# Kernel tuning notes

Hardware: AMD Instinct MI355X
Metric: run time of the kernel (lower is better)

The kernel has to match this reference:

```python
import jax, jax.numpy as jnp
import numpy as np

N, E, IN_DIM, HID, PROJ, NG = 50000, 1600000, 128, 128, 128, 64


def setup_inputs() -> dict:
    key = jax.random.key(0)
    ks = jax.random.split(key, 12)
    def glorot(k, fan_in, fan_out):
        s = (6.0 / (fan_in + fan_out)) ** 0.5
        return jax.random.uniform(k, (fan_in, fan_out), jnp.float32, -s, s)
    x = jax.random.normal(ks[0], (N, IN_DIM), jnp.float32)
    edge_index = jax.random.randint(ks[1], (2, E), 0, N, jnp.int32)
    batch = jnp.sort(jax.random.randint(ks[2], (N,), 0, NG, jnp.int32))
    return {
        "x": x,
        "edge_index": edge_index,
        "batch": batch,
        "num_graphs": NG,
        "W1": glorot(ks[3], IN_DIM, HID), "b1": jnp.zeros((HID,), jnp.float32),
        "W2": glorot(ks[4], HID, HID),    "b2": jnp.zeros((HID,), jnp.float32),
        "pW1": glorot(ks[5], HID, HID),   "pb1": jnp.zeros((HID,), jnp.float32),
        "pW2": glorot(ks[6], HID, PROJ),  "pb2": jnp.zeros((PROJ,), jnp.float32),
    }


def _gcn_norm(edge_index, n_nodes):
    # add self loops, compute symmetric normalization (PyG GCNConv default)
    loop = jnp.arange(n_nodes, dtype=edge_index.dtype)
    src = jnp.concatenate([edge_index[0], loop])
    dst = jnp.concatenate([edge_index[1], loop])
    deg = jax.ops.segment_sum(jnp.ones_like(dst, jnp.float32), dst, num_segments=n_nodes)
    dinv = jnp.where(deg > 0, jax.lax.rsqrt(deg), 0.0)
    norm = dinv[src] * dinv[dst]  # [E+N]
    return src, dst, norm


def _gcn_conv(h, W, b, src, dst, norm, n_nodes):
    hw = h @ W                              # [N, out]
    msg = hw[src] * norm[:, None]           # gather + scale, [E+N, out]
    out = jax.ops.segment_sum(msg, dst, num_segments=n_nodes)  # scatter-add
    return out + b


def reference(x, edge_index, batch, num_graphs, W1, b1, W2, b2, pW1, pb1, pW2, pb2):
    n_nodes = x.shape[0]
    src, dst, norm = _gcn_norm(edge_index, n_nodes)
    # conv stack (dropout is identity in eval mode)
    h = jax.nn.relu(_gcn_conv(x, W1, b1, src, dst, norm, n_nodes))
    h = jax.nn.relu(_gcn_conv(h, W2, b2, src, dst, norm, n_nodes))
    # global mean pool over graphs
    sums = jax.ops.segment_sum(h, batch, num_segments=num_graphs)
    cnts = jax.ops.segment_sum(jnp.ones((n_nodes,), h.dtype), batch, num_segments=num_graphs)
    hg = sums / jnp.maximum(cnts, 1.0)[:, None]
    # MLP projection head
    z = jax.nn.relu(hg @ pW1 + pb1) @ pW2 + pb2
    # L2 normalize (torch F.normalize with eps=1e-12)
    nrm = jnp.maximum(jnp.linalg.norm(z, axis=1, keepdims=True), 1e-12)
    return z / nrm
```

## Files before the change

### kernel.cpp

```cpp
#include <hip/hip_runtime.h>
#include <cstdint>
#include <cstddef>


using short8 = __attribute__((ext_vector_type(8))) short;
using f32x4v = __attribute__((ext_vector_type(4))) float;


static __device__ __forceinline__ unsigned f2bf_rne(float f) {
    unsigned u = __float_as_uint(f);
    return (u + 0x7FFFu + ((u >> 16) & 1u)) >> 16;
}
static __device__ __forceinline__ unsigned pack_bf2(float lo, float hi) {
    return f2bf_rne(lo) | (f2bf_rne(hi) << 16);
}
static __device__ __forceinline__ float bf_lo(unsigned v) {
    return __uint_as_float(v << 16);
}
static __device__ __forceinline__ float bf_hi(unsigned v) {
    return __uint_as_float(v & 0xFFFF0000u);
}


__global__ void k_bincount(const int* __restrict__ dst, int* __restrict__ bcnt,
                           int E, int NB) {
    __shared__ int h[256];
    int t = threadIdx.x;
    h[t] = 0;
    __syncthreads();
    int base_i = blockIdx.x * 4096;
#pragma unroll
    for (int j = 0; j < 16; ++j) {
        int i = base_i + j * 256 + t;
        if (i < E) atomicAdd(&h[dst[i] >> 8], 1);
    }
    __syncthreads();
    if (t < NB && h[t]) atomicAdd(&bcnt[t], h[t]);
}

__global__ void k_bscan(const int* __restrict__ bcnt, int* __restrict__ bbase,
                        int* __restrict__ bcur, int NB,
                        float* __restrict__ pooled, int* __restrict__ cnt,
                        unsigned* __restrict__ hwdummy, int NG) {
    __shared__ int s[256];
    int t = threadIdx.x;
    int v = (t < NB) ? bcnt[t] : 0;
    s[t] = v;
    __syncthreads();
    for (int d = 1; d < 256; d <<= 1) {
        int x = (t >= d) ? s[t - d] : 0;
        __syncthreads();
        s[t] += x;
        __syncthreads();
    }
    if (t < NB) {
        int excl = s[t] - v;
        bbase[t] = excl;
        bcur[t]  = excl;
        if (t == NB - 1) bbase[NB] = s[t];
    }
    float4 z4 = {0.f, 0.f, 0.f, 0.f};
    int n4 = NG * 32;
    for (int i = t; i < n4; i += 256)
        reinterpret_cast<float4*>(pooled)[i] = z4;
    if (t < NG) cnt[t] = 0;
    if (t < 64) hwdummy[t] = 0u;
}


__global__ void k_bin(const int* __restrict__ src, const int* __restrict__ dst,
                      int* __restrict__ bcur, int* __restrict__ bkt,
                      int E, int NB) {
    __shared__ int cnt[256];
    __shared__ int pos[256];
    int t = threadIdx.x;
    int base_i = blockIdx.x * 4096;

    cnt[t] = 0;
    __syncthreads();

    int b_[16];
    int v_[16];
#pragma unroll
    for (int j = 0; j < 16; ++j) {
        int i = base_i + j * 256 + t;
        if (i < E) {
            int s = src[i], d = dst[i];
            v_[j] = s | ((d & 255) << 16);
            int b = d >> 8;
            b_[j] = b;
            atomicAdd(&cnt[b], 1);
        } else {
            b_[j] = -1;
        }
    }
    __syncthreads();

    if (t < NB) {
        int c = cnt[t];
        pos[t] = c ? atomicAdd(&bcur[t], c) : 0;
    }
    __syncthreads();

#pragma unroll
    for (int j = 0; j < 16; ++j) {
        if (b_[j] >= 0) {
            int p = atomicAdd(&pos[b_[j]], 1);
            bkt[p] = v_[j];
        }
    }
}


__global__ void k_fill2(const int* __restrict__ bkt, const int* __restrict__ bbase,
                        int* __restrict__ off, float* __restrict__ dinv,
                        int* __restrict__ csr, int N, int E, int NB) {
    __shared__ int hist[256];
    __shared__ int loff[256];
    __shared__ int cur[256];
    int b = blockIdx.x, t = threadIdx.x;
    if (t < 256) hist[t] = 0;
    __syncthreads();

    int e0 = bbase[b], e1 = bbase[b + 1];
    for (int i = e0 + t; i < e1; i += 1024)
        atomicAdd(&hist[(bkt[i] >> 16) & 255], 1);
    __syncthreads();

    if (t < 256) loff[t] = hist[t];
    __syncthreads();
    for (int d = 1; d < 256; d <<= 1) {
        int x = 0;
        if (t < 256 && t >= d) x = loff[t - d];
        __syncthreads();
        if (t < 256) loff[t] += x;
        __syncthreads();
    }

    if (t < 256) {
        int n = (b << 8) + t;
        if (n < N) {
            int base = e0 + loff[t] - hist[t];
            off[n]  = base;
            cur[t]  = base;
            dinv[n] = rsqrtf((float)(hist[t] + 1));
        }
    }
    if (b == NB - 1 && t == 0) off[N] = E;
    __syncthreads();

    for (int i = e0 + t; i < e1; i += 1024) {
        int v  = bkt[i];
        int dl = (v >> 16) & 255;
        int p  = atomicAdd(&cur[dl], 1);
        csr[p] = v & 0xFFFF;
    }
}


template<bool BF16IN>
__global__ __launch_bounds__(256) void k_gemm(
        const void* __restrict__ in_, const float* __restrict__ W,
        const float* __restrict__ dinv, unsigned* __restrict__ outbf, int N) {
    __shared__ unsigned short wbf[128 * 136];

    int t = threadIdx.x;
    int w  = t >> 6;
    int l  = t & 63;
    int lo = l & 15;
    int hi = l >> 4;

#pragma unroll
    for (int i = 0; i < 16; ++i) {
        int idx = (i * 256 + t) * 4;
        float4 wv = *reinterpret_cast<const float4*>(W + idx);
        int k = idx >> 7, c = idx & 127;
        wbf[(c    ) * 136 + k] = (unsigned short)f2bf_rne(wv.x);
        wbf[(c + 1) * 136 + k] = (unsigned short)f2bf_rne(wv.y);
        wbf[(c + 2) * 136 + k] = (unsigned short)f2bf_rne(wv.z);
        wbf[(c + 3) * 136 + k] = (unsigned short)f2bf_rne(wv.w);
    }
    __syncthreads();

    unsigned short* outS = (unsigned short*)outbf;

#pragma unroll
    for (int tt = 0; tt < 2; ++tt) {
        int rbase = (blockIdx.x * 2 + tt) * 64 + w * 16;
        if (rbase >= N) continue;
        int row  = rbase + lo;
        int rowc = (row < N) ? row : (N - 1);

        short8 a[4];
        if constexpr (BF16IN) {
            const uint4* pu = (const uint4*)in_;
#pragma unroll
            for (int ks = 0; ks < 4; ++ks)
                a[ks] = __builtin_bit_cast(short8, pu[(size_t)rowc * 16 + ks * 4 + hi]);
        } else {
            const float4* pf = (const float4*)in_;
#pragma unroll
            for (int ks = 0; ks < 4; ++ks) {
                float4 fA = pf[(size_t)rowc * 32 + ks * 8 + hi * 2];
                float4 fB = pf[(size_t)rowc * 32 + ks * 8 + hi * 2 + 1];
                short8 s;
                s[0] = (short)f2bf_rne(fA.x); s[1] = (short)f2bf_rne(fA.y);
                s[2] = (short)f2bf_rne(fA.z); s[3] = (short)f2bf_rne(fA.w);
                s[4] = (short)f2bf_rne(fB.x); s[5] = (short)f2bf_rne(fB.y);
                s[6] = (short)f2bf_rne(fB.z); s[7] = (short)f2bf_rne(fB.w);
                a[ks] = s;
            }
        }

        f32x4v acc[8];
#pragma unroll
        for (int i = 0; i < 8; ++i) acc[i] = (f32x4v){0.f, 0.f, 0.f, 0.f};

#pragma unroll
        for (int cp = 0; cp < 2; ++cp) {
            short8 b[4][4];
#pragma unroll
            for (int ct = 0; ct < 4; ++ct) {
                int col = cp * 64 + ct * 16 + lo;
#pragma unroll
                for (int ks = 0; ks < 4; ++ks)
                    b[ct][ks] = *reinterpret_cast<const short8*>(
                        &wbf[col * 136 + ks * 32 + hi * 8]);
            }
#pragma unroll
            for (int ks = 0; ks < 4; ++ks)
#pragma unroll
                for (int ct = 0; ct < 4; ++ct)
                    acc[cp * 4 + ct] = __builtin_amdgcn_mfma_f32_16x16x32_bf16(
                        b[ct][ks], a[ks], acc[cp * 4 + ct], 0, 0, 0);
        }

        if (row < N) {
            float d = dinv[row];
#pragma unroll
            for (int i = 0; i < 8; ++i) {
                int colb = (i >> 2) * 64 + (i & 3) * 16 + hi * 4;
                uint2 o = { pack_bf2(acc[i][0] * d, acc[i][1] * d),
                            pack_bf2(acc[i][2] * d, acc[i][3] * d) };
                *reinterpret_cast<uint2*>(&outS[(size_t)row * 128 + colb]) = o;
            }
        }
    }
}


__global__ void k_aggr(const unsigned* __restrict__ hw, const int* __restrict__ off,
                       const int* __restrict__ csr, const float* __restrict__ dinv,
                       const float* __restrict__ bias, unsigned* __restrict__ out, int N) {
    int wid  = (blockIdx.x * blockDim.x + threadIdx.x) >> 6;
    int lane = threadIdx.x & 63;
    if (wid >= N) return;
    int n  = wid;
    int q  = lane >> 4;
    int li = lane & 15;

    const uint4* hw4 = reinterpret_cast<const uint4*>(hw);

    float a0 = 0.f, a1 = 0.f, a2 = 0.f, a3 = 0.f;
    float a4 = 0.f, a5 = 0.f, a6 = 0.f, a7 = 0.f;
    if (q == 0) {
        uint4 v = hw4[(unsigned)(n << 4) + li];
        a0 = bf_lo(v.x); a1 = bf_hi(v.x);
        a2 = bf_lo(v.y); a3 = bf_hi(v.y);
        a4 = bf_lo(v.z); a5 = bf_hi(v.z);
        a6 = bf_lo(v.w); a7 = bf_hi(v.w);
    }

#define ACC8(v) \
    a0 += bf_lo(v.x); a1 += bf_hi(v.x); \
    a2 += bf_lo(v.y); a3 += bf_hi(v.y); \
    a4 += bf_lo(v.z); a5 += bf_hi(v.z); \
    a6 += bf_lo(v.w); a7 += bf_hi(v.w);

    int e = off[n], e1 = off[n + 1];
    while (e < e1) {
        int rem = e1 - e;
        int cnt = rem < 64 ? rem : 64;
        int s_l = N;
        if (lane < cnt) s_l = csr[e + lane];
        int jn = (cnt + 3) >> 2;
        int j = 0;
        for (; j + 8 <= jn; j += 8) {
            int s0 = __shfl(s_l, 4 * j + q);
            int s1 = __shfl(s_l, 4 * j + 4 + q);
            int s2 = __shfl(s_l, 4 * j + 8 + q);
            int s3 = __shfl(s_l, 4 * j + 12 + q);
            int s4 = __shfl(s_l, 4 * j + 16 + q);
            int s5 = __shfl(s_l, 4 * j + 20 + q);
            int s6 = __shfl(s_l, 4 * j + 24 + q);
            int s7 = __shfl(s_l, 4 * j + 28 + q);
            uint4 v0 = hw4[(unsigned)(s0 << 4) + li];
            uint4 v1 = hw4[(unsigned)(s1 << 4) + li];
            uint4 v2 = hw4[(unsigned)(s2 << 4) + li];
            uint4 v3 = hw4[(unsigned)(s3 << 4) + li];
            uint4 v4 = hw4[(unsigned)(s4 << 4) + li];
            uint4 v5 = hw4[(unsigned)(s5 << 4) + li];
            uint4 v6 = hw4[(unsigned)(s6 << 4) + li];
            uint4 v7 = hw4[(unsigned)(s7 << 4) + li];
            ACC8(v0) ACC8(v1) ACC8(v2) ACC8(v3)
            ACC8(v4) ACC8(v5) ACC8(v6) ACC8(v7)
        }
        for (; j + 4 <= jn; j += 4) {
            int s0 = __shfl(s_l, 4 * j + q);
            int s1 = __shfl(s_l, 4 * j + 4 + q);
            int s2 = __shfl(s_l, 4 * j + 8 + q);
            int s3 = __shfl(s_l, 4 * j + 12 + q);
            uint4 v0 = hw4[(unsigned)(s0 << 4) + li];
            uint4 v1 = hw4[(unsigned)(s1 << 4) + li];
            uint4 v2 = hw4[(unsigned)(s2 << 4) + li];
            uint4 v3 = hw4[(unsigned)(s3 << 4) + li];
            ACC8(v0) ACC8(v1) ACC8(v2) ACC8(v3)
        }
        for (; j < jn; ++j) {
            int   s = __shfl(s_l, 4 * j + q);
            uint4 v = hw4[(unsigned)(s << 4) + li];
            ACC8(v)
        }
        e += cnt;
    }
#undef ACC8

    int p1 = (lane + 32) & 63;
    a0 += __shfl(a0, p1); a1 += __shfl(a1, p1);
    a2 += __shfl(a2, p1); a3 += __shfl(a3, p1);
    a4 += __shfl(a4, p1); a5 += __shfl(a5, p1);
    a6 += __shfl(a6, p1); a7 += __shfl(a7, p1);
    int p2 = (lane + 16) & 63;
    a0 += __shfl(a0, p2); a1 += __shfl(a1, p2);
    a2 += __shfl(a2, p2); a3 += __shfl(a3, p2);
    a4 += __shfl(a4, p2); a5 += __shfl(a5, p2);
    a6 += __shfl(a6, p2); a7 += __shfl(a7, p2);

    if (q == 0) {
        float di = dinv[n];
        const float4* b4 = reinterpret_cast<const float4*>(bias);
        float4 bA = b4[2 * li], bB = b4[2 * li + 1];
        a0 = fmaxf(fmaf(a0, di, bA.x), 0.f); a1 = fmaxf(fmaf(a1, di, bA.y), 0.f);
        a2 = fmaxf(fmaf(a2, di, bA.z), 0.f); a3 = fmaxf(fmaf(a3, di, bA.w), 0.f);
        a4 = fmaxf(fmaf(a4, di, bB.x), 0.f); a5 = fmaxf(fmaf(a5, di, bB.y), 0.f);
        a6 = fmaxf(fmaf(a6, di, bB.z), 0.f); a7 = fmaxf(fmaf(a7, di, bB.w), 0.f);
        uint4 r = { pack_bf2(a0, a1), pack_bf2(a2, a3),
                    pack_bf2(a4, a5), pack_bf2(a6, a7) };
        reinterpret_cast<uint4*>(out)[(unsigned)(n << 4) + li] = r;
    }
}


__global__ void k_pool(const unsigned* __restrict__ h, const int* __restrict__ batch,
                       float* __restrict__ pooled, int* __restrict__ cnt,
                       int N, int npw) {
    int wid  = (blockIdx.x * blockDim.x + threadIdx.x) >> 6;
    int lane = threadIdx.x & 63;
    int n0 = wid * npw;
    if (n0 >= N) return;
    int n1 = n0 + npw; if (n1 > N) n1 = N;

    float ax = 0.f, ay = 0.f;
    int g = batch[n0];
    int c = 0;
    for (int n = n0; n < n1; ++n) {
        int gn = batch[n];
        if (gn != g) {
            atomicAdd(&pooled[g * 128 + 2 * lane],     ax);
            atomicAdd(&pooled[g * 128 + 2 * lane + 1], ay);
            if (lane == 0) atomicAdd(&cnt[g], c);
            ax = 0.f; ay = 0.f; c = 0; g = gn;
        }
        unsigned v = h[(size_t)n * 64 + lane];
        ax += bf_lo(v); ay += bf_hi(v); ++c;
    }
    atomicAdd(&pooled[g * 128 + 2 * lane],     ax);
    atomicAdd(&pooled[g * 128 + 2 * lane + 1], ay);
    if (lane == 0) atomicAdd(&cnt[g], c);
}


__global__ void k_head(const float* __restrict__ pooled, const int* __restrict__ cnt,
                       const float* __restrict__ pW1, const float* __restrict__ pb1,
                       const float* __restrict__ pW2, const float* __restrict__ pb2,
                       float* __restrict__ out) {
    __shared__ float hg[128];
    __shared__ float z1[128];
    __shared__ float red[128];
    int g = blockIdx.x, t = threadIdx.x;

    float c = fmaxf((float)cnt[g], 1.0f);
    hg[t] = pooled[g * 128 + t] / c;
    __syncthreads();

    float a = pb1[t];
#pragma unroll 8
    for (int k = 0; k < 128; ++k) a = fmaf(hg[k], pW1[k * 128 + t], a);
    z1[t] = fmaxf(a, 0.f);
    __syncthreads();

    float z = pb2[t];
#pragma unroll 8
    for (int k = 0; k < 128; ++k) z = fmaf(z1[k], pW2[k * 128 + t], z);

    red[t] = z * z;
    __syncthreads();
    for (int d = 64; d > 0; d >>= 1) {
        if (t < d) red[t] += red[t + d];
        __syncthreads();
    }
    float nrm = fmaxf(sqrtf(red[0]), 1e-12f);
    out[g * 128 + t] = z / nrm;
}


extern "C" void kernel_launch(void* const* d_in, const int* in_sizes, int n_in,
                              void* d_out, int out_size, void* d_ws, size_t ws_size,
                              hipStream_t stream) {
    const float* x    = (const float*)d_in[0];
    const int*   eidx = (const int*)  d_in[1];
    const int*   batch= (const int*)  d_in[2];
    const float* W1   = (const float*)d_in[4];
    const float* b1   = (const float*)d_in[5];
    const float* W2   = (const float*)d_in[6];
    const float* b2   = (const float*)d_in[7];
    const float* pW1  = (const float*)d_in[8];
    const float* pb1  = (const float*)d_in[9];
    const float* pW2  = (const float*)d_in[10];
    const float* pb2  = (const float*)d_in[11];
    float* out = (float*)d_out;

    const int N  = in_sizes[0] / 128;
    const int E  = in_sizes[1] / 2;
    const int NG = out_size / 128;
    const int NB = (N + 255) >> 8;

    const int* src = eidx;
    const int* dst = eidx + E;

    char* p = (char*)d_ws;
    auto alloc = [&](size_t bytes) -> void* {
        void* r = (void*)p;
        p += (bytes + 255) & ~(size_t)255;
        return r;
    };
    int*      bcnt     = (int*)     alloc((size_t)NB * 4);
    int*      cnt      = (int*)     alloc((size_t)NG * 4);
    float*    pooled   = (float*)   alloc((size_t)NG * 128 * 4);
    int*      bbase    = (int*)     alloc((size_t)(NB + 1) * 4);
    int*      bcur     = (int*)     alloc((size_t)NB * 4);
    int*      off      = (int*)     alloc((size_t)(N + 1) * 4);
    float*    dinv     = (float*)   alloc((size_t)N * 4);
    int*      bkt      = (int*)     alloc((size_t)E * 4);
    int*      csr      = (int*)     alloc((size_t)E * 4);
    unsigned* bufH     = (unsigned*)alloc((size_t)(N + 1) * 64 * 4);
    unsigned* bufB     = (unsigned*)alloc((size_t)N * 64 * 4);
    (void)ws_size;

    const int tB = (E + 4095) / 4096;

    hipMemsetAsync(bcnt, 0, (size_t)NB * 4, stream);

    k_bincount<<<tB, 256, 0, stream>>>(dst, bcnt, E, NB);
    k_bscan   <<<1, 256, 0, stream>>>(bcnt, bbase, bcur, NB,
                                      pooled, cnt, bufH + (size_t)N * 64, NG);
    k_bin     <<<tB, 256, 0, stream>>>(src, dst, bcur, bkt, E, NB);
    k_fill2   <<<NB, 1024, 0, stream>>>(bkt, bbase, off, dinv, csr, N, E, NB);

    const int nrt = (N + 63) / 64;
    const int gB  = (nrt + 1) / 2;
    const int aB  = (N + 3) / 4;

    k_gemm<false><<<gB, 256, 0, stream>>>((const void*)x, W1, dinv, bufH, N);
    k_aggr<<<aB, 256, 0, stream>>>(bufH, off, csr, dinv, b1, bufB, N);
    k_gemm<true><<<gB, 256, 0, stream>>>((const void*)bufB, W2, dinv, bufH, N);
    k_aggr<<<aB, 256, 0, stream>>>(bufH, off, csr, dinv, b2, bufB, N);

    const int NPW = 32;
    const int waves = (N + NPW - 1) / NPW;
    const int pB = (waves * 64 + 255) / 256;
    k_pool<<<pB, 256, 0, stream>>>(bufB, batch, pooled, cnt, N, NPW);

    k_head<<<NG, 128, 0, stream>>>(pooled, cnt, pW1, pb1, pW2, pb2, out);
}
```

Measured before the change: 220.9 us.

## Privatize per-wave LDS histograms and fuse mean pooling into head kernel

The binning, bucket-fill and CSR-fill kernels now give each wave (or each 256-thread group) its own shared-memory histogram and cursor array, to reduce contention on shared atomics. The pooling kernel and its zero-initialisation are removed. Each head block now binary-searches the sorted batch array for its graph's node range and sums that range itself, with no global float atomics and one fewer launch. In exchange, pooling runs on only 64 blocks, each walking about 780 nodes serially, which may expose memory latency. The fused path also assumes batch is sorted.

```diff
diff --git a/kernel.cpp b/kernel.cpp
--- a/kernel.cpp
+++ b/kernel.cpp
@@ -24,24 +24,30 @@
 
 __global__ void k_bincount(const int* __restrict__ dst, int* __restrict__ bcnt,
                            int E, int NB) {
-    __shared__ int h[256];
+    __shared__ int h4[4][256];
     int t = threadIdx.x;
-    h[t] = 0;
+    int w = t >> 6;
+    ((int*)h4)[t]       = 0;
+    ((int*)h4)[t + 256] = 0;
+    ((int*)h4)[t + 512] = 0;
+    ((int*)h4)[t + 768] = 0;
     __syncthreads();
     int base_i = blockIdx.x * 4096;
 #pragma unroll
     for (int j = 0; j < 16; ++j) {
         int i = base_i + j * 256 + t;
-        if (i < E) atomicAdd(&h[dst[i] >> 8], 1);
-    }
-    __syncthreads();
-    if (t < NB && h[t]) atomicAdd(&bcnt[t], h[t]);
+        if (i < E) atomicAdd(&h4[w][dst[i] >> 8], 1);
+    }
+    __syncthreads();
+    if (t < NB) {
+        int s = h4[0][t] + h4[1][t] + h4[2][t] + h4[3][t];
+        if (s) atomicAdd(&bcnt[t], s);
+    }
 }
 
 __global__ void k_bscan(const int* __restrict__ bcnt, int* __restrict__ bbase,
                         int* __restrict__ bcur, int NB,
-                        float* __restrict__ pooled, int* __restrict__ cnt,
-                        unsigned* __restrict__ hwdummy, int NG) {
+                        unsigned* __restrict__ hwdummy) {
     __shared__ int s[256];
     int t = threadIdx.x;
     int v = (t < NB) ? bcnt[t] : 0;
@@ -59,11 +65,6 @@
         bcur[t]  = excl;
         if (t == NB - 1) bbase[NB] = s[t];
     }
-    float4 z4 = {0.f, 0.f, 0.f, 0.f};
-    int n4 = NG * 32;
-    for (int i = t; i < n4; i += 256)
-        reinterpret_cast<float4*>(pooled)[i] = z4;
-    if (t < NG) cnt[t] = 0;
     if (t < 64) hwdummy[t] = 0u;
 }
 
@@ -71,14 +72,17 @@
 __global__ void k_bin(const int* __restrict__ src, const int* __restrict__ dst,
                       int* __restrict__ bcur, int* __restrict__ bkt,
                       int E, int NB) {
-    __shared__ int cnt[256];
-    __shared__ int pos[256];
+    __shared__ int h4[4][256];
+    __shared__ int pw[4][256];
     int t = threadIdx.x;
+    int w = t >> 6;
+    ((int*)h4)[t]       = 0;
+    ((int*)h4)[t + 256] = 0;
+    ((int*)h4)[t + 512] = 0;
+    ((int*)h4)[t + 768] = 0;
+    __syncthreads();
+
     int base_i = blockIdx.x * 4096;
-
-    cnt[t] = 0;
-    __syncthreads();
-
     int b_[16];
     int v_[16];
 #pragma unroll
@@ -89,7 +93,7 @@
             v_[j] = s | ((d & 255) << 16);
             int b = d >> 8;
             b_[j] = b;
-            atomicAdd(&cnt[b], 1);
+            atomicAdd(&h4[w][b], 1);
         } else {
             b_[j] = -1;
         }
@@ -97,15 +101,20 @@
     __syncthreads();
 
     if (t < NB) {
-        int c = cnt[t];
-        pos[t] = c ? atomicAdd(&bcur[t], c) : 0;
+        int c0 = h4[0][t], c1 = h4[1][t], c2 = h4[2][t], c3 = h4[3][t];
+        int tot = c0 + c1 + c2 + c3;
+        int base = tot ? atomicAdd(&bcur[t], tot) : 0;
+        pw[0][t] = base;
+        pw[1][t] = base + c0;
+        pw[2][t] = base + c0 + c1;
+        pw[3][t] = base + c0 + c1 + c2;
     }
     __syncthreads();
 
 #pragma unroll
     for (int j = 0; j < 16; ++j) {
         if (b_[j] >= 0) {
-            int p = atomicAdd(&pos[b_[j]], 1);
+            int p = atomicAdd(&pw[w][b_[j]], 1);
             bkt[p] = v_[j];
         }
     }
@@ -115,19 +124,24 @@
 __global__ void k_fill2(const int* __restrict__ bkt, const int* __restrict__ bbase,
                         int* __restrict__ off, float* __restrict__ dinv,
                         int* __restrict__ csr, int N, int E, int NB) {
-    __shared__ int hist[256];
+    __shared__ int h4[4][256];
     __shared__ int loff[256];
-    __shared__ int cur[256];
+    __shared__ int cur4[4][256];
     int b = blockIdx.x, t = threadIdx.x;
-    if (t < 256) hist[t] = 0;
+    int grp = t >> 8;
+    ((int*)h4)[t] = 0;
     __syncthreads();
 
     int e0 = bbase[b], e1 = bbase[b + 1];
     for (int i = e0 + t; i < e1; i += 1024)
-        atomicAdd(&hist[(bkt[i] >> 16) & 255], 1);
-    __syncthreads();
-
-    if (t < 256) loff[t] = hist[t];
+        atomicAdd(&h4[grp][(bkt[i] >> 16) & 255], 1);
+    __syncthreads();
+
+    int tot = 0;
+    if (t < 256) {
+        tot = h4[0][t] + h4[1][t] + h4[2][t] + h4[3][t];
+        loff[t] = tot;
+    }
     __syncthreads();
     for (int d = 1; d < 256; d <<= 1) {
         int x = 0;
@@ -140,10 +154,13 @@
     if (t < 256) {
         int n = (b << 8) + t;
         if (n < N) {
-            int base = e0 + loff[t] - hist[t];
+            int base = e0 + loff[t] - tot;
             off[n]  = base;
-            cur[t]  = base;
-            dinv[n] = rsqrtf((float)(hist[t] + 1));
+            dinv[n] = rsqrtf((float)(tot + 1));
+            cur4[0][t] = base;
+            cur4[1][t] = base + h4[0][t];
+            cur4[2][t] = base + h4[0][t] + h4[1][t];
+            cur4[3][t] = base + h4[0][t] + h4[1][t] + h4[2][t];
         }
     }
     if (b == NB - 1 && t == 0) off[N] = E;
@@ -152,7 +169,7 @@
     for (int i = e0 + t; i < e1; i += 1024) {
         int v  = bkt[i];
         int dl = (v >> 16) & 255;
-        int p  = atomicAdd(&cur[dl], 1);
+        int p  = atomicAdd(&cur4[grp][dl], 1);
         csr[p] = v & 0xFFFF;
     }
 }
@@ -351,36 +368,8 @@
 }
 
 
-__global__ void k_pool(const unsigned* __restrict__ h, const int* __restrict__ batch,
-                       float* __restrict__ pooled, int* __restrict__ cnt,
-                       int N, int npw) {
-    int wid  = (blockIdx.x * blockDim.x + threadIdx.x) >> 6;
-    int lane = threadIdx.x & 63;
-    int n0 = wid * npw;
-    if (n0 >= N) return;
-    int n1 = n0 + npw; if (n1 > N) n1 = N;
-
-    float ax = 0.f, ay = 0.f;
-    int g = batch[n0];
-    int c = 0;
-    for (int n = n0; n < n1; ++n) {
-        int gn = batch[n];
-        if (gn != g) {
-            atomicAdd(&pooled[g * 128 + 2 * lane],     ax);
-            atomicAdd(&pooled[g * 128 + 2 * lane + 1], ay);
-            if (lane == 0) atomicAdd(&cnt[g], c);
-            ax = 0.f; ay = 0.f; c = 0; g = gn;
-        }
-        unsigned v = h[(size_t)n * 64 + lane];
-        ax += bf_lo(v); ay += bf_hi(v); ++c;
-    }
-    atomicAdd(&pooled[g * 128 + 2 * lane],     ax);
-    atomicAdd(&pooled[g * 128 + 2 * lane + 1], ay);
-    if (lane == 0) atomicAdd(&cnt[g], c);
-}
-
-
-__global__ void k_head(const float* __restrict__ pooled, const int* __restrict__ cnt,
+__global__ void k_head(const unsigned* __restrict__ h, const int* __restrict__ batch,
+                       int N,
                        const float* __restrict__ pW1, const float* __restrict__ pb1,
                        const float* __restrict__ pW2, const float* __restrict__ pb2,
                        float* __restrict__ out) {
@@ -389,8 +378,22 @@
     __shared__ float red[128];
     int g = blockIdx.x, t = threadIdx.x;
 
-    float c = fmaxf((float)cnt[g], 1.0f);
-    hg[t] = pooled[g * 128 + t] / c;
+    int lo = 0, hi = N;
+    while (lo < hi) { int m = (lo + hi) >> 1; if (batch[m] < g) lo = m + 1; else hi = m; }
+    int start = lo;
+    hi = N;
+    while (lo < hi) { int m = (lo + hi) >> 1; if (batch[m] < g + 1) lo = m + 1; else hi = m; }
+    int end = lo;
+
+    int  ui   = t >> 1;
+    bool hiH  = t & 1;
+    float acc = 0.f;
+    for (int n = start; n < end; ++n) {
+        unsigned v = h[(size_t)n * 64 + ui];
+        acc += hiH ? bf_hi(v) : bf_lo(v);
+    }
+    float c = fmaxf((float)(end - start), 1.0f);
+    hg[t] = acc / c;
     __syncthreads();
 
     float a = pb1[t];
@@ -445,8 +448,6 @@
         return r;
     };
     int*      bcnt     = (int*)     alloc((size_t)NB * 4);
-    int*      cnt      = (int*)     alloc((size_t)NG * 4);
-    float*    pooled   = (float*)   alloc((size_t)NG * 128 * 4);
     int*      bbase    = (int*)     alloc((size_t)(NB + 1) * 4);
     int*      bcur     = (int*)     alloc((size_t)NB * 4);
     int*      off      = (int*)     alloc((size_t)(N + 1) * 4);
@@ -463,7 +464,7 @@
 
     k_bincount<<<tB, 256, 0, stream>>>(dst, bcnt, E, NB);
     k_bscan   <<<1, 256, 0, stream>>>(bcnt, bbase, bcur, NB,
-                                      pooled, cnt, bufH + (size_t)N * 64, NG);
+                                      bufH + (size_t)N * 64);
     k_bin     <<<tB, 256, 0, stream>>>(src, dst, bcur, bkt, E, NB);
     k_fill2   <<<NB, 1024, 0, stream>>>(bkt, bbase, off, dinv, csr, N, E, NB);
 
@@ -476,10 +477,5 @@
     k_gemm<true><<<gB, 256, 0, stream>>>((const void*)bufB, W2, dinv, bufH, N);
     k_aggr<<<aB, 256, 0, stream>>>(bufH, off, csr, dinv, b2, bufB, N);
 
-    const int NPW = 32;
-    const int waves = (N + NPW - 1) / NPW;
-    const int pB = (waves * 64 + 255) / 256;
-    k_pool<<<pB, 256, 0, stream>>>(bufB, batch, pooled, cnt, N, NPW);
-
-    k_head<<<NG, 128, 0, stream>>>(pooled, cnt, pW1, pb1, pW2, pb2, out);
-}
+    k_head<<<NG, 128, 0, stream>>>(bufB, batch, N, pW1, pb1, pW2, pb2, out);
+}
```

After: 410.6 us. 1.86x slower.
